# Kernel optimization log

Hardware: AMD Instinct MI355X
Metric: run time of the kernel (lower is better)

## Reference

```python
import jax, jax.numpy as jnp
import numpy as np
from jax import lax

B, D, H, W, C = 2, 144, 64, 160, 32
P = 300000
EPS = 1e-4   # scn BatchNormLeakyReLU default eps
LEAK = 0.2


def setup_inputs() -> dict:
    key = jax.random.key(0)
    ks = jax.random.split(key, 10)
    features = jax.random.normal(ks[0], (P, C), jnp.float32)
    b = jax.random.randint(ks[1], (P, 1), 0, B)
    x = jax.random.randint(ks[2], (P, 1), 0, D)
    y = jax.random.randint(ks[3], (P, 1), 0, H)
    z = jax.random.randint(ks[4], (P, 1), 0, W)
    coords = jnp.concatenate([b, x, y, z], axis=1).astype(jnp.int32)

    def conv_w(k, cin, cout):
        return jax.random.normal(k, (2, 2, 2, cin, cout), jnp.float32) / np.float32(np.sqrt(8 * cin))

    return {
        "features": features, "coords": coords,
        "w1": conv_w(ks[5], C, 64),  "g1": jnp.ones((64,), jnp.float32),  "b1": jnp.zeros((64,), jnp.float32),
        "w2": conv_w(ks[6], 64, 96), "g2": jnp.ones((96,), jnp.float32),  "b2": jnp.zeros((96,), jnp.float32),
        "w3": conv_w(ks[7], 96, 128),"g3": jnp.ones((128,), jnp.float32), "b3": jnp.zeros((128,), jnp.float32),
        "w4": conv_w(ks[8], 128, 1),
    }


def _densify(features, coords):
    # scn.InputLayer mode=4: average features of duplicate coordinates.
    lin = ((coords[:, 0] * D + coords[:, 1]) * H + coords[:, 2]) * W + coords[:, 3]
    grid = jnp.zeros((B * D * H * W, C), features.dtype).at[lin].add(features)
    cnt = jnp.zeros((B * D * H * W,), features.dtype).at[lin].add(1.0)
    grid = grid / jnp.maximum(cnt, 1.0)[:, None]
    x = grid.reshape(B, D, H, W, C)
    mask = (cnt > 0).astype(features.dtype).reshape(B, D, H, W, 1)
    return x, mask


def _conv2s2(x, w):
    # scn.Convolution(dim=3, filter=2, stride=2, bias=False): inactive inputs are zero,
    # so dense VALID conv reproduces values at active output sites exactly.
    return lax.conv_general_dilated(x, w, (2, 2, 2), 'VALID',
                                    dimension_numbers=('NDHWC', 'DHWIO', 'NDHWC'))


def _downsample_mask(mask):
    # Output site is active iff any input in its 2x2x2 window is active.
    return lax.reduce_window(mask, 0.0, lax.max, (1, 2, 2, 2, 1), (1, 2, 2, 2, 1), 'VALID')


def _block(x, mask, w, gamma, beta):
    x = _conv2s2(x, w)
    mask = _downsample_mask(mask)
    n = jnp.maximum(jnp.sum(mask), 1.0)
    # x is exactly zero at inactive sites, so sums over all sites == sums over active sites.
    mean = jnp.sum(x, axis=(0, 1, 2, 3)) / n
    var = jnp.sum(x * x, axis=(0, 1, 2, 3)) / n - mean * mean
    y = (x - mean) * (gamma * lax.rsqrt(var + EPS)) + beta
    y = jnp.where(y > 0, y, LEAK * y) * mask   # LeakyReLU on active sites, zero elsewhere
    return y, mask


def reference(features, coords, w1, g1, b1, w2, g2, b2, w3, g3, b3, w4):
    x, mask = _densify(features, coords)
    x, mask = _block(x, mask, w1, g1, b1)
    x, mask = _block(x, mask, w2, g2, b2)
    x, mask = _block(x, mask, w3, g3, b3)
    x = _conv2s2(x, w4)                 # [B, 9, 4, 10, 1]
    mask = _downsample_mask(mask)
    return jax.nn.sigmoid(x) * mask     # sigmoid of features; inactive sites zeroed
```

## Files before the change

kernel.cpp:

```cpp
#include <hip/hip_runtime.h>
#include <math.h>

#define PNUM 300000
#define B_ 2
#define D0 144
#define H0 64
#define W0 160
#define NVOX (B_*D0*H0*W0)

#define D1 72
#define H1 32
#define W1 80
#define N1S (B_*D1*H1*W1)

#define D2 36
#define H2 16
#define W2 40
#define N2S (B_*D2*H2*W2)

#define D3 18
#define H3 8
#define W3 20
#define N3S (B_*D3*H3*W3)

#define D4 9
#define H4 4
#define W4 10
#define N4S (B_*D4*H4*W4)

#define EPS_ 1e-4f
#define LEAK_ 0.2f

typedef __attribute__((ext_vector_type(8))) short v8s;
typedef __attribute__((ext_vector_type(4))) float v4f;

typedef unsigned short ushort_t;
typedef unsigned int uint_t;
typedef unsigned long long ull_t;

__device__ __forceinline__ ushort_t f2b(float f) {
  union { float f; uint_t u; } x; x.f = f;
  uint_t r = x.u + 0x7FFFu + ((x.u >> 16) & 1u);
  return (ushort_t)(r >> 16);
}
__device__ __forceinline__ float b2f(ushort_t h) {
  union { uint_t u; float f; } x; x.u = ((uint_t)h) << 16; return x.f;
}
__device__ __forceinline__ uint_t bn2(uint_t w, float s0, float h0, float s1, float h1,
                                      float msk) {
  float v0 = b2f((ushort_t)(w & 0xffff));
  float v1 = b2f((ushort_t)(w >> 16));
  v0 = fmaf(v0, s0, h0); v1 = fmaf(v1, s1, h1);
  v0 = fmaxf(v0, LEAK_ * v0) * msk;
  v1 = fmaxf(v1, LEAK_ * v1) * msk;
  return (uint_t)f2b(v0) | ((uint_t)f2b(v1) << 16);
}

#define OFF_CNT     0
#define OFF_STATS   2949120
#define OFF_START   2965504
#define OFF_SORTED  5914624
#define OFF_AKLIST  6214624
#define OFF_WT1     6514624
#define OFF_WT2     6522816
#define OFF_WT3     6555584
#define OFF_AFEATB  6621120
#define OFF_X1B     11421120
#define OFF_X2B     23217600
#define OFF_X3B     26166720
#define OFF_M1      26535360
#define OFF_M2      26904000
#define OFF_M3      26950080

#define ST_S1P  0
#define ST_Q1P  2560
#define ST_S2P  5120
#define ST_Q2P  7424
#define ST_S3P  9728
#define ST_Q3P  12032
#define ST_N2P  14336
#define ST_N3P  14368
#define ST_GCUR 14400
#define ST_PK   14404

__device__ __forceinline__ int voxkey(int b, int x, int y, int z) {
  int p = ((b*D1 + (x >> 1))*H1 + (y >> 1))*W1 + (z >> 1);
  int oct = ((x & 1) << 2) | ((y & 1) << 1) | (z & 1);
  return p*8 + oct;
}

__global__ __launch_bounds__(256) void k_count(const int* __restrict__ coords,
                                               int* __restrict__ cnt) {
  int i = blockIdx.x * 256 + threadIdx.x;
  if (i >= PNUM) return;
  int4 c = *(const int4*)(coords + i*4);
  atomicAdd(&cnt[voxkey(c.x, c.y, c.z, c.w)], 1);
}

__global__ __launch_bounds__(1024) void k_alloc(const int* __restrict__ cnt,
                                                int* __restrict__ start,
                                                int* __restrict__ cursor,
                                                int* __restrict__ gcur) {
  __shared__ int wsum[16];
  __shared__ int blockBase;
  int t = threadIdx.x;
  int idx0 = blockIdx.x * 16384 + t * 16;
  int c[16];
  int tsum = 0;
#pragma unroll
  for (int j = 0; j < 4; j++) {
    int4 cv = *(const int4*)(cnt + idx0 + j*4);
    c[j*4+0] = cv.x; c[j*4+1] = cv.y; c[j*4+2] = cv.z; c[j*4+3] = cv.w;
    tsum += cv.x + cv.y + cv.z + cv.w;
  }
  int lane = t & 63, wid = t >> 6;
  int incl = tsum;
#pragma unroll
  for (int off = 1; off < 64; off <<= 1) {
    int v = __shfl_up(incl, off);
    if (lane >= off) incl += v;
  }
  if (lane == 63) wsum[wid] = incl;
  __syncthreads();
  if (t == 0) {
    int tot = 0;
#pragma unroll
    for (int w = 0; w < 16; w++) { int v = wsum[w]; wsum[w] = tot; tot += v; }
    blockBase = atomicAdd(gcur, tot);
  }
  __syncthreads();
  int st = blockBase + wsum[wid] + incl - tsum;
#pragma unroll
  for (int j = 0; j < 4; j++) {
    int4 sv;
    sv.x = st; st += c[j*4+0];
    sv.y = st; st += c[j*4+1];
    sv.z = st; st += c[j*4+2];
    sv.w = st; st += c[j*4+3];
    *(int4*)(start + idx0 + j*4) = sv;
    *(int4*)(cursor + idx0 + j*4) = sv;
  }
}

__global__ __launch_bounds__(256) void k_scatter(const int* __restrict__ coords,
                                                 int* __restrict__ cursor,
                                                 int* __restrict__ sorted) {
  int i = blockIdx.x * 256 + threadIdx.x;
  if (i >= PNUM) return;
  int4 c = *(const int4*)(coords + i*4);
  int slot = atomicAdd(&cursor[voxkey(c.x, c.y, c.z, c.w)], 1);
  sorted[slot] = i;
}

__global__ __launch_bounds__(1024) void k_plist(const int* __restrict__ cnt,
                                                float* __restrict__ m1,
                                                int* __restrict__ aklist,
                                                ull_t* __restrict__ pkctr) {
  __shared__ int wsum[16];
  __shared__ ull_t sbase;
  int t = threadIdx.x;
  int p0 = blockIdx.x * 4096 + t * 4;
  int lane = t & 63, wid = t >> 6;
  uint_t mb[4];
  int packed = 0;
#pragma unroll
  for (int j = 0; j < 4; j++) {
    const int4* c4 = (const int4*)(cnt + (size_t)(p0 + j)*8);
    int4 a = c4[0], b = c4[1];
    uint_t m = 0;
    m |= (a.x > 0) ? 1u : 0; m |= (a.y > 0) ? 2u : 0;
    m |= (a.z > 0) ? 4u : 0; m |= (a.w > 0) ? 8u : 0;
    m |= (b.x > 0) ? 16u : 0; m |= (b.y > 0) ? 32u : 0;
    m |= (b.z > 0) ? 64u : 0; m |= (b.w > 0) ? 128u : 0;
    mb[j] = m;
    int ck = __popc(m);
    int pa = (ck > 0) ? 1 : 0;
    m1[p0 + j] = pa ? 1.f : 0.f;
    packed += (pa << 16) | ck;
  }
  int incl = packed;
#pragma unroll
  for (int o = 1; o < 64; o <<= 1) {
    int v = __shfl_up(incl, o);
    if (lane >= o) incl += v;
  }
  if (lane == 63) wsum[wid] = incl;
  __syncthreads();
  if (t == 0) {
    int tot = 0;
#pragma unroll
    for (int w = 0; w < 16; w++) { int v = wsum[w]; wsum[w] = tot; tot += v; }
    ull_t add = ((ull_t)(uint_t)(tot >> 16) << 32) | (ull_t)(uint_t)(tot & 0xffff);
    sbase = atomicAdd(pkctr, add);
  }
  __syncthreads();
  ull_t base = sbase;
  int excl = wsum[wid] + incl - packed;
  int koff = (int)(base & 0xffffffffULL) + (excl & 0xffff);
#pragma unroll
  for (int j = 0; j < 4; j++) {
    uint_t m = mb[j];
    while (m) {
      int i = __ffs(m) - 1; m &= m - 1;
      aklist[koff++] = (p0 + j)*8 + i;
    }
  }
}

__global__ __launch_bounds__(256) void k_avg(const float* __restrict__ feat,
                                             const int* __restrict__ sorted,
                                             const int* __restrict__ cnt,
                                             const int* __restrict__ start,
                                             const int* __restrict__ aklist,
                                             const int* __restrict__ nactk,
                                             ushort_t* __restrict__ afb) {
  int gid = blockIdx.x * 256 + threadIdx.x;
  int j = gid >> 3;
  if (j >= nactk[0]) return;
  int key = aklist[j];
  int c = cnt[key];
  int s0 = start[key];
  int q = (gid & 7) * 4;
  float4 acc = {0.f, 0.f, 0.f, 0.f};
  for (int i = 0; i < c; i++) {
    float4 v = *(const float4*)(feat + (size_t)sorted[s0 + i] * 32 + q);
    acc.x += v.x; acc.y += v.y; acc.z += v.z; acc.w += v.w;
  }
  float inv = 1.f / (float)c;
  uint2 o;
  o.x = (uint_t)f2b(acc.x*inv) | ((uint_t)f2b(acc.y*inv) << 16);
  o.y = (uint_t)f2b(acc.z*inv) | ((uint_t)f2b(acc.w*inv) << 16);
  *(uint2*)(afb + (size_t)s0 * 32 + q) = o;
}

__global__ __launch_bounds__(256) void k_prepw(const float* __restrict__ w1,
                                               const float* __restrict__ w2,
                                               const float* __restrict__ w3,
                                               ushort_t* __restrict__ wt1,
                                               ushort_t* __restrict__ wt2,
                                               ushort_t* __restrict__ wt3) {
  int idx = blockIdx.x * 256 + threadIdx.x;
  if (idx < 16384) {
    int c = idx >> 11, r = idx & 2047;
    int co = r >> 5, kk = r & 31;
    wt1[idx] = f2b(w1[(c*32 + kk)*64 + co]);
  } else if (idx < 16384 + 65536) {
    int i = idx - 16384;
    int c = i >> 12, r = i & 4095;
    int co = r >> 5, kk = r & 31;
    int k = c*32 + kk;
    wt2[i] = (co < 96) ? f2b(w2[k*96 + co]) : 0;
  } else if (idx < 16384 + 65536 + 131072) {
    int i = idx - 81920;
    int c = i >> 12, r = i & 4095;
    int co = r >> 5, kk = r & 31;
    int k = c*32 + kk;
    int ch = k >> 7, ci = k & 127;
    wt3[i] = (ci < 96) ? f2b(w3[(ch*96 + ci)*128 + co]) : 0;
  }
}

__global__ __launch_bounds__(256) void k_conv1m(
    const ushort_t* __restrict__ afb, const int* __restrict__ cnt,
    const int* __restrict__ start, const ushort_t* __restrict__ wtg,
    ushort_t* __restrict__ x1b, float* __restrict__ sp, float* __restrict__ qp) {
  __shared__ __align__(16) ushort_t wlds[16384];
  __shared__ int cst[128*9];
  __shared__ float redS[4][64], redQ[4][64];
  int t = threadIdx.x;
#pragma unroll
  for (int i = 0; i < 8; i++)
    ((uint4*)wlds)[t + i*256] = ((const uint4*)wtg)[t + i*256];
  if (t < 128) {
    int p = blockIdx.x * 128 + t;
    const int4* cp = (const int4*)(cnt + (size_t)p*8);
    const int4* spt = (const int4*)(start + (size_t)p*8);
    int4 c0 = cp[0], c1 = cp[1], s0 = spt[0], s1 = spt[1];
    cst[t*9 + 0] = (c0.x > 0) ? s0.x : -1;
    cst[t*9 + 1] = (c0.y > 0) ? s0.y : -1;
    cst[t*9 + 2] = (c0.z > 0) ? s0.z : -1;
    cst[t*9 + 3] = (c0.w > 0) ? s0.w : -1;
    cst[t*9 + 4] = (c1.x > 0) ? s1.x : -1;
    cst[t*9 + 5] = (c1.y > 0) ? s1.y : -1;
    cst[t*9 + 6] = (c1.z > 0) ? s1.z : -1;
    cst[t*9 + 7] = (c1.w > 0) ? s1.w : -1;
  }
  __syncthreads();
  int lane = t & 63, wv = t >> 6;
  int l15 = lane & 15, q = lane >> 4;
  int SB = wv * 32;
  v8s a[8][2];
#pragma unroll
  for (int c = 0; c < 8; c++) {
#pragma unroll
    for (int mt = 0; mt < 2; mt++) {
      int site = SB + mt*16 + l15;
      int sp2 = cst[site*9 + c];
      v8s av = {0,0,0,0,0,0,0,0};
      if (sp2 >= 0) av = *(const v8s*)(afb + (size_t)sp2*32 + q*8);
      a[c][mt] = av;
    }
  }
  v4f acc[2][4];
#pragma unroll
  for (int i = 0; i < 2; i++)
#pragma unroll
    for (int j = 0; j < 4; j++) acc[i][j] = (v4f){0.f, 0.f, 0.f, 0.f};
#pragma unroll
  for (int c = 0; c < 8; c++) {
    v8s b[4];
#pragma unroll
    for (int nt = 0; nt < 4; nt++)
      b[nt] = *(const v8s*)&wlds[c*2048 + (nt*16 + l15)*32 + q*8];
#pragma unroll
    for (int mt = 0; mt < 2; mt++)
#pragma unroll
      for (int nt = 0; nt < 4; nt++)
        acc[mt][nt] = __builtin_amdgcn_mfma_f32_16x16x32_bf16(a[c][mt], b[nt], acc[mt][nt], 0, 0, 0);
  }
  int pbase = blockIdx.x * 128;
  float ss[4] = {0,0,0,0}, sq[4] = {0,0,0,0};
#pragma unroll
  for (int mt = 0; mt < 2; mt++) {
#pragma unroll
    for (int nt = 0; nt < 4; nt++) {
#pragma unroll
      for (int r = 0; r < 4; r++) {
        int sl = SB + mt*16 + q*4 + r;
        ushort_t h = f2b(acc[mt][nt][r]);
        float v = b2f(h);
        x1b[(size_t)(pbase + sl)*64 + nt*16 + l15] = h;
        ss[nt] += v; sq[nt] += v*v;
      }
    }
  }
#pragma unroll
  for (int nt = 0; nt < 4; nt++) {
    float v1 = ss[nt], v2 = sq[nt];
    v1 += __shfl_xor(v1, 16); v1 += __shfl_xor(v1, 32);
    v2 += __shfl_xor(v2, 16); v2 += __shfl_xor(v2, 32);
    if (lane < 16) { redS[wv][nt*16 + l15] = v1; redQ[wv][nt*16 + l15] = v2; }
  }
  __syncthreads();
  if (t < 64) {
    float s = redS[0][t] + redS[1][t] + redS[2][t] + redS[3][t];
    float qq = redQ[0][t] + redQ[1][t] + redQ[2][t] + redQ[3][t];
    int row = (blockIdx.x & 31) * 80;
    atomicAdd(&sp[row + t], s);
    atomicAdd(&qp[row + t], qq);
  }
}

template <int CSTRIDE, int CIN_REAL, bool NINT, int NROW, int INSTR,
          int DO, int HO, int WO, int DP, int HP, int WP>
__global__ __launch_bounds__(256) void k_convm(
    const ushort_t* __restrict__ xin, const float* __restrict__ mprev,
    const ushort_t* __restrict__ wtg,
    const float* __restrict__ gam, const float* __restrict__ bet,
    const float* __restrict__ spin, const float* __restrict__ qpin,
    const void* __restrict__ ncnt, const float* __restrict__ npin,
    ushort_t* __restrict__ xout, float* __restrict__ osum, float* __restrict__ osq,
    float* __restrict__ mout, float* __restrict__ npart) {
  const int NCHUNK = CSTRIDE / 4;
  __shared__ __align__(16) float sc[CSTRIDE], sh[CSTRIDE];
  __shared__ int   cbase[64*9];
  __shared__ float cmask[64*9];
  __shared__ float redS[4][64], redQ[4][64];
  int t = threadIdx.x;
  if (t < CSTRIDE) {
    float scv = 0.f, shv = 0.f;
    if (t < CIN_REAL) {
      float n;
      if (NINT) n = fmaxf((float)((const int*)ncnt)[0], 1.0f);
      else {
        float nn = 0.f;
        for (int r = 0; r < 32; r++) nn += npin[r];
        n = fmaxf(nn, 1.0f);
      }
      float s1 = 0.f, q1 = 0.f;
      for (int r = 0; r < NROW; r++) { s1 += spin[r*INSTR + t]; q1 += qpin[r*INSTR + t]; }
      float mean = s1 / n;
      float var = q1 / n - mean * mean;
      float s = gam[t] * rsqrtf(var + EPS_);
      scv = s; shv = bet[t] - mean * s;
    }
    sc[t] = scv; sh[t] = shv;
  }
#pragma unroll
  for (int ii = 0; ii < 2; ii++) {
    int idx = t + ii*256;
    int s = idx >> 3, ch = idx & 7;
    int g = blockIdx.x * 64 + s;
    int b = g / (DO*HO*WO); int r = g - b*(DO*HO*WO);
    int ox = r / (HO*WO); r -= ox*(HO*WO);
    int oy = r / WO; int oz = r - oy*WO;
    int ps = ((b*DP + 2*ox + ((ch >> 2) & 1))*HP + 2*oy + ((ch >> 1) & 1))*WP + 2*oz + (ch & 1);
    cbase[s*9 + ch] = ps * CSTRIDE;
    cmask[s*9 + ch] = mprev[ps];
  }
  __syncthreads();
  int lane = t & 63, wv = t >> 6;
  int l15 = lane & 15, q = lane >> 4;
  int SB = (wv & 1) * 32, NB = (wv >> 1) * 64;
  v4f acc[2][4];
#pragma unroll
  for (int i = 0; i < 2; i++)
#pragma unroll
    for (int j = 0; j < 4; j++) acc[i][j] = (v4f){0.f, 0.f, 0.f, 0.f};
  uint4 rawN[2]; float mskN[2]; v8s bN[4];
#pragma unroll
  for (int mt = 0; mt < 2; mt++) {
    int site = SB + mt*16 + l15;
    rawN[mt] = *(const uint4*)(xin + (size_t)cbase[site*9] + q*8);
    mskN[mt] = cmask[site*9];
  }
#pragma unroll
  for (int nt = 0; nt < 4; nt++)
    bN[nt] = *(const v8s*)(wtg + (NB + nt*16 + l15)*32 + q*8);
#pragma unroll
  for (int c = 0; c < NCHUNK; c++) {
    uint4 raw[2] = {rawN[0], rawN[1]};
    float mskc[2] = {mskN[0], mskN[1]};
    v8s b[4] = {bN[0], bN[1], bN[2], bN[3]};
    if (c + 1 < NCHUNK) {
      int ch1 = ((c+1) * 32) / CSTRIDE;
      int cio1 = ((c+1) * 32) % CSTRIDE + q * 8;
#pragma unroll
      for (int mt = 0; mt < 2; mt++) {
        int site = SB + mt*16 + l15;
        rawN[mt] = *(const uint4*)(xin + (size_t)cbase[site*9 + ch1] + cio1);
        mskN[mt] = cmask[site*9 + ch1];
      }
#pragma unroll
      for (int nt = 0; nt < 4; nt++)
        bN[nt] = *(const v8s*)(wtg + (size_t)(c+1)*4096 + (NB + nt*16 + l15)*32 + q*8);
    }
    int cio = (c * 32) % CSTRIDE + q * 8;
    float4 sc0 = *(const float4*)&sc[cio];
    float4 sc1 = *(const float4*)&sc[cio + 4];
    float4 sh0 = *(const float4*)&sh[cio];
    float4 sh1 = *(const float4*)&sh[cio + 4];
    v8s a[2];
#pragma unroll
    for (int mt = 0; mt < 2; mt++) {
      int4 pk;
      pk.x = (int)bn2(raw[mt].x, sc0.x, sh0.x, sc0.y, sh0.y, mskc[mt]);
      pk.y = (int)bn2(raw[mt].y, sc0.z, sh0.z, sc0.w, sh0.w, mskc[mt]);
      pk.z = (int)bn2(raw[mt].z, sc1.x, sh1.x, sc1.y, sh1.y, mskc[mt]);
      pk.w = (int)bn2(raw[mt].w, sc1.z, sh1.z, sc1.w, sh1.w, mskc[mt]);
      a[mt] = *(v8s*)&pk;
    }
#pragma unroll
    for (int mt = 0; mt < 2; mt++)
#pragma unroll
      for (int nt = 0; nt < 4; nt++)
        acc[mt][nt] = __builtin_amdgcn_mfma_f32_16x16x32_bf16(a[mt], b[nt], acc[mt][nt], 0, 0, 0);
  }
  float ss[4] = {0,0,0,0}, sq[4] = {0,0,0,0};
#pragma unroll
  for (int mt = 0; mt < 2; mt++) {
#pragma unroll
    for (int nt = 0; nt < 4; nt++) {
#pragma unroll
      for (int r = 0; r < 4; r++) {
        int sl = SB + mt*16 + q*4 + r;
        size_t gsite = (size_t)blockIdx.x * 64 + sl;
        ushort_t h = f2b(acc[mt][nt][r]);
        float v = b2f(h);
        xout[gsite*128 + NB + nt*16 + l15] = h;
        ss[nt] += v; sq[nt] += v*v;
      }
    }
  }
  if (t < 64) {
    bool act = false;
#pragma unroll
    for (int ch = 0; ch < 8; ch++) act |= (cmask[t*9 + ch] > 0.f);
    mout[blockIdx.x * 64 + t] = act ? 1.f : 0.f;
    unsigned long long bal = __ballot(act);
    if (t == 0) atomicAdd(&npart[blockIdx.x & 31], (float)__popcll(bal));
  }
#pragma unroll
  for (int nt = 0; nt < 4; nt++) {
    float v1 = ss[nt], v2 = sq[nt];
    v1 += __shfl_xor(v1, 16); v1 += __shfl_xor(v1, 32);
    v2 += __shfl_xor(v2, 16); v2 += __shfl_xor(v2, 32);
    if (lane < 16) { redS[wv][nt*16 + l15] = v1; redQ[wv][nt*16 + l15] = v2; }
  }
  __syncthreads();
  if (t < 128) {
    float s, qq;
    if (t < 64) { s = redS[0][t] + redS[1][t]; qq = redQ[0][t] + redQ[1][t]; }
    else        { s = redS[2][t-64] + redS[3][t-64]; qq = redQ[2][t-64] + redQ[3][t-64]; }
    int row = (blockIdx.x & 15) * 144;
    atomicAdd(&osum[row + t], s);
    atomicAdd(&osq[row + t], qq);
  }
}

__global__ __launch_bounds__(256) void k_final(
    const ushort_t* __restrict__ x3b, const float* __restrict__ m3,
    const float* __restrict__ w4, const float* __restrict__ gam,
    const float* __restrict__ bet, const float* __restrict__ spin,
    const float* __restrict__ qpin, const float* __restrict__ npin,
    float* __restrict__ out) {
  __shared__ float sc[128], sh[128];
  __shared__ int cb[8];
  __shared__ float msk[8];
  __shared__ float red[256];
  int t = threadIdx.x;
  if (t < 128) {
    float nn = 0.f;
    for (int r = 0; r < 32; r++) nn += npin[r];
    float n = fmaxf(nn, 1.0f);
    float s1 = 0.f, q1 = 0.f;
    for (int r = 0; r < 16; r++) { s1 += spin[r*144 + t]; q1 += qpin[r*144 + t]; }
    float mean = s1 / n;
    float var = q1 / n - mean * mean;
    float s = gam[t] * rsqrtf(var + EPS_);
    sc[t] = s; sh[t] = bet[t] - mean * s;
  }
  int g = blockIdx.x;
  int b = g / (D4*H4*W4); int r = g - b*(D4*H4*W4);
  int ox = r / (H4*W4); r -= ox*(H4*W4);
  int oy = r / W4; int oz = r - oy*W4;
  if (t < 8) {
    int ps = ((b*D3 + 2*ox + ((t >> 2) & 1))*H3 + 2*oy + ((t >> 1) & 1))*W3 + 2*oz + (t & 1);
    cb[t] = ps * 128;
    msk[t] = m3[ps];
  }
  __syncthreads();
  float acc = 0.f;
#pragma unroll
  for (int ii = 0; ii < 4; ii++) {
    int k = t + ii*256;
    int ch = k >> 7, ci = k & 127;
    float v = b2f(x3b[cb[ch] + ci]);
    v = v * sc[ci] + sh[ci];
    v = (v > 0.f ? v : LEAK_ * v) * msk[ch];
    acc += v * w4[k];
  }
  red[t] = acc;
  __syncthreads();
  if (t < 128) red[t] += red[t + 128];
  __syncthreads();
  if (t < 64) {
    float v = red[t] + red[t + 64];
#pragma unroll
    for (int off = 32; off > 0; off >>= 1) v += __shfl_down(v, off);
    if (t == 0) {
      float any = (msk[0] + msk[1] + msk[2] + msk[3] + msk[4] + msk[5] + msk[6] + msk[7]) > 0.f ? 1.f : 0.f;
      out[g] = any / (1.0f + expf(-v));
    }
  }
}

extern "C" void kernel_launch(void* const* d_in, const int* in_sizes, int n_in,
                              void* d_out, int out_size, void* d_ws, size_t ws_size,
                              hipStream_t stream) {
  (void)in_sizes; (void)n_in; (void)out_size; (void)ws_size;
  const float* feat = (const float*)d_in[0];
  const int*   crd  = (const int*)d_in[1];
  const float* w1 = (const float*)d_in[2];
  const float* g1 = (const float*)d_in[3];
  const float* b1 = (const float*)d_in[4];
  const float* w2 = (const float*)d_in[5];
  const float* g2 = (const float*)d_in[6];
  const float* b2 = (const float*)d_in[7];
  const float* w3 = (const float*)d_in[8];
  const float* g3 = (const float*)d_in[9];
  const float* b3 = (const float*)d_in[10];
  const float* w4 = (const float*)d_in[11];
  float* out = (float*)d_out;
  float* ws  = (float*)d_ws;

  int*      cnt    = (int*)(ws + OFF_CNT);
  float*    st     = ws + OFF_STATS;
  int*      start  = (int*)(ws + OFF_START);
  int*      sorted = (int*)(ws + OFF_SORTED);
  int*      aklist = (int*)(ws + OFF_AKLIST);
  ushort_t* wt1g   = (ushort_t*)(ws + OFF_WT1);
  ushort_t* wt2g   = (ushort_t*)(ws + OFF_WT2);
  ushort_t* wt3g   = (ushort_t*)(ws + OFF_WT3);
  ushort_t* afb    = (ushort_t*)(ws + OFF_AFEATB);
  ushort_t* x1b    = (ushort_t*)(ws + OFF_X1B);
  int*      cursor = (int*)(ws + OFF_X1B);
  ushort_t* x2b    = (ushort_t*)(ws + OFF_X2B);
  ushort_t* x3b    = (ushort_t*)(ws + OFF_X3B);
  float*    m1     = ws + OFF_M1;
  float*    m2     = ws + OFF_M2;
  float*    m3     = ws + OFF_M3;
  ull_t*    pkctr  = (ull_t*)(st + ST_PK);
  int*      nactk  = (int*)(st + ST_PK);
  int*      nactp  = (int*)(st + ST_PK + 1);

  hipMemsetAsync(d_ws, 0, (size_t)(OFF_STATS + 16384) * sizeof(float), stream);

  k_count<<<(PNUM + 255) / 256, 256, 0, stream>>>(crd, cnt);
  k_alloc<<<NVOX / 16384, 1024, 0, stream>>>(cnt, start, cursor, (int*)(st + ST_GCUR));
  k_scatter<<<(PNUM + 255) / 256, 256, 0, stream>>>(crd, cursor, sorted);
  k_plist<<<N1S / 4096, 1024, 0, stream>>>(cnt, m1, aklist, pkctr);
  k_avg<<<(PNUM * 8) / 256 + 1, 256, 0, stream>>>(feat, sorted, cnt, start, aklist,
                                                  nactk, afb);
  k_prepw<<<(16384 + 65536 + 131072) / 256, 256, 0, stream>>>(w1, w2, w3, wt1g, wt2g, wt3g);
  k_conv1m<<<N1S / 128, 256, 0, stream>>>(afb, cnt, start, wt1g, x1b,
                                          st + ST_S1P, st + ST_Q1P);
  k_convm<64, 64, true, 32, 80, D2,H2,W2, D1,H1,W1><<<N2S / 64, 256, 0, stream>>>(
      x1b, m1, wt2g, g1, b1, st + ST_S1P, st + ST_Q1P, (const void*)nactp, nullptr,
      x2b, st + ST_S2P, st + ST_Q2P, m2, st + ST_N2P);
  k_convm<128, 96, false, 16, 144, D3,H3,W3, D2,H2,W2><<<N3S / 64, 256, 0, stream>>>(
      x2b, m2, wt3g, g2, b2, st + ST_S2P, st + ST_Q2P, nullptr, st + ST_N2P,
      x3b, st + ST_S3P, st + ST_Q3P, m3, st + ST_N3P);
  k_final<<<N4S, 256, 0, stream>>>(x3b, m3, w4, g3, b3,
                                   st + ST_S3P, st + ST_Q3P, st + ST_N3P, out);
}
```

Before: 255.8 us.

## Store intermediate grids in octant-blocked order and fuse front-end kernels

Each level's output is now written in octant-blocked (Morton-like) order, so the next conv's 2x2x2 window inputs sit contiguously. That removes the per-site index division and gathered base computation, and makes the input loads contiguous. The active-list build is folded into the allocation scan, count/weight-prep/stats-zeroing are merged into one launch, and the start array is dropped in favour of cursor minus count. The cost is scattered output stores through okey remapping and a 64-bit packed scan in k_alloc.

```diff
diff --git a/kernel.cpp b/kernel.cpp
--- a/kernel.cpp
+++ b/kernel.cpp
@@ -56,9 +56,18 @@
   return (uint_t)f2b(v0) | ((uint_t)f2b(v1) << 16);
 }
 
+template <int DD, int HH, int WW>
+__device__ __forceinline__ int okey(int p) {
+  int b = p / (DD*HH*WW); int r = p - b*(DD*HH*WW);
+  int x = r / (HH*WW); r -= x*(HH*WW);
+  int y = r / WW; int z = r - y*WW;
+  return (((((b*(DD/2) + (x >> 1))*(HH/2) + (y >> 1))*(WW/2)) + (z >> 1)) << 3)
+         | ((x & 1) << 2) | ((y & 1) << 1) | (z & 1);
+}
+
 #define OFF_CNT     0
 #define OFF_STATS   2949120
-#define OFF_START   2965504
+#define OFF_CURSOR  2965504
 #define OFF_SORTED  5914624
 #define OFF_AKLIST  6214624
 #define OFF_WT1     6514624
@@ -89,20 +98,57 @@
   return p*8 + oct;
 }
 
-__global__ __launch_bounds__(256) void k_count(const int* __restrict__ coords,
-                                               int* __restrict__ cnt) {
-  int i = blockIdx.x * 256 + threadIdx.x;
-  if (i >= PNUM) return;
-  int4 c = *(const int4*)(coords + i*4);
-  atomicAdd(&cnt[voxkey(c.x, c.y, c.z, c.w)], 1);
+#define NB_COUNT 1172
+#define NB_PREPW 832
+#define NB_STZ   16
+__global__ __launch_bounds__(256) void k_front(
+    const int* __restrict__ coords, int* __restrict__ cnt,
+    const float* __restrict__ w1, const float* __restrict__ w2,
+    const float* __restrict__ w3,
+    ushort_t* __restrict__ wt1, ushort_t* __restrict__ wt2,
+    ushort_t* __restrict__ wt3, float* __restrict__ stz) {
+  int bb = blockIdx.x, t = threadIdx.x;
+  if (bb < NB_COUNT) {
+    int i = bb * 256 + t;
+    if (i < PNUM) {
+      int4 c = *(const int4*)(coords + i*4);
+      atomicAdd(&cnt[voxkey(c.x, c.y, c.z, c.w)], 1);
+    }
+  } else if (bb < NB_COUNT + NB_PREPW) {
+    int idx = (bb - NB_COUNT) * 256 + t;
+    if (idx < 16384) {
+      int c = idx >> 11, r = idx & 2047;
+      int co = r >> 5, kk = r & 31;
+      wt1[idx] = f2b(w1[(c*32 + kk)*64 + co]);
+    } else if (idx < 16384 + 65536) {
+      int i = idx - 16384;
+      int c = i >> 12, r = i & 4095;
+      int co = r >> 5, kk = r & 31;
+      int k = c*32 + kk;
+      wt2[i] = (co < 96) ? f2b(w2[k*96 + co]) : 0;
+    } else {
+      int i = idx - 81920;
+      int c = i >> 12, r = i & 4095;
+      int co = r >> 5, kk = r & 31;
+      int k = c*32 + kk;
+      int ch = k >> 7, ci = k & 127;
+      wt3[i] = (ci < 96) ? f2b(w3[(ch*96 + ci)*128 + co]) : 0;
+    }
+  } else {
+    int off = ((bb - NB_COUNT - NB_PREPW) * 256 + t) * 4;
+    *(float4*)(stz + off) = make_float4(0.f, 0.f, 0.f, 0.f);
+  }
 }
 
 __global__ __launch_bounds__(1024) void k_alloc(const int* __restrict__ cnt,
-                                                int* __restrict__ start,
                                                 int* __restrict__ cursor,
-                                                int* __restrict__ gcur) {
-  __shared__ int wsum[16];
-  __shared__ int blockBase;
+                                                float* __restrict__ m1b,
+                                                int* __restrict__ aklist,
+                                                int* __restrict__ gcur,
+                                                ull_t* __restrict__ pkctr) {
+  __shared__ ull_t wsum[16];
+  __shared__ int slotBase;
+  __shared__ ull_t pkBase;
   int t = threadIdx.x;
   int idx0 = blockIdx.x * 16384 + t * 16;
   int c[16];
@@ -113,33 +159,52 @@
     c[j*4+0] = cv.x; c[j*4+1] = cv.y; c[j*4+2] = cv.z; c[j*4+3] = cv.w;
     tsum += cv.x + cv.y + cv.z + cv.w;
   }
+  uint_t m0 = 0, m1m = 0;
+#pragma unroll
+  for (int j = 0; j < 8; j++) { if (c[j] > 0) m0 |= (1u << j); }
+#pragma unroll
+  for (int j = 0; j < 8; j++) { if (c[8+j] > 0) m1m |= (1u << j); }
+  int ck = __popc(m0) + __popc(m1m);
+  int pa = ((m0 != 0) ? 1 : 0) + ((m1m != 0) ? 1 : 0);
+  ull_t sv = ((ull_t)(uint_t)tsum << 32) | (ull_t)(uint_t)((pa << 16) | ck);
   int lane = t & 63, wid = t >> 6;
-  int incl = tsum;
-#pragma unroll
-  for (int off = 1; off < 64; off <<= 1) {
-    int v = __shfl_up(incl, off);
-    if (lane >= off) incl += v;
+  ull_t incl = sv;
+#pragma unroll
+  for (int o = 1; o < 64; o <<= 1) {
+    ull_t v = __shfl_up(incl, o);
+    if (lane >= o) incl += v;
   }
   if (lane == 63) wsum[wid] = incl;
   __syncthreads();
   if (t == 0) {
-    int tot = 0;
-#pragma unroll
-    for (int w = 0; w < 16; w++) { int v = wsum[w]; wsum[w] = tot; tot += v; }
-    blockBase = atomicAdd(gcur, tot);
-  }
-  __syncthreads();
-  int st = blockBase + wsum[wid] + incl - tsum;
+    ull_t tot = 0;
+#pragma unroll
+    for (int w = 0; w < 16; w++) { ull_t v = wsum[w]; wsum[w] = tot; tot += v; }
+    slotBase = atomicAdd(gcur, (int)(tot >> 32));
+    uint_t pk = (uint_t)(tot & 0xffffffffULL);
+    pkBase = atomicAdd(pkctr, ((ull_t)(pk >> 16) << 32) | (ull_t)(pk & 0xffff));
+  }
+  __syncthreads();
+  ull_t excl = wsum[wid] + incl - sv;
+  int st = slotBase + (int)(excl >> 32);
+  uint_t pkl = (uint_t)(excl & 0xffffffffULL);
+  int koff = (int)(pkBase & 0xffffffffULL) + (int)(pkl & 0xffff);
 #pragma unroll
   for (int j = 0; j < 4; j++) {
-    int4 sv;
-    sv.x = st; st += c[j*4+0];
-    sv.y = st; st += c[j*4+1];
-    sv.z = st; st += c[j*4+2];
-    sv.w = st; st += c[j*4+3];
-    *(int4*)(start + idx0 + j*4) = sv;
-    *(int4*)(cursor + idx0 + j*4) = sv;
-  }
+    int4 sv2;
+    sv2.x = st; st += c[j*4+0];
+    sv2.y = st; st += c[j*4+1];
+    sv2.z = st; st += c[j*4+2];
+    sv2.w = st; st += c[j*4+3];
+    *(int4*)(cursor + idx0 + j*4) = sv2;
+  }
+  int p0 = idx0 >> 3;
+  m1b[okey<D1,H1,W1>(p0)]     = (m0 != 0) ? 1.f : 0.f;
+  m1b[okey<D1,H1,W1>(p0 + 1)] = (m1m != 0) ? 1.f : 0.f;
+  uint_t m = m0;
+  while (m) { int i = __ffs(m) - 1; m &= m - 1; aklist[koff++] = p0*8 + i; }
+  m = m1m;
+  while (m) { int i = __ffs(m) - 1; m &= m - 1; aklist[koff++] = (p0 + 1)*8 + i; }
 }
 
 __global__ __launch_bounds__(256) void k_scatter(const int* __restrict__ coords,
@@ -152,65 +217,10 @@
   sorted[slot] = i;
 }
 
-__global__ __launch_bounds__(1024) void k_plist(const int* __restrict__ cnt,
-                                                float* __restrict__ m1,
-                                                int* __restrict__ aklist,
-                                                ull_t* __restrict__ pkctr) {
-  __shared__ int wsum[16];
-  __shared__ ull_t sbase;
-  int t = threadIdx.x;
-  int p0 = blockIdx.x * 4096 + t * 4;
-  int lane = t & 63, wid = t >> 6;
-  uint_t mb[4];
-  int packed = 0;
-#pragma unroll
-  for (int j = 0; j < 4; j++) {
-    const int4* c4 = (const int4*)(cnt + (size_t)(p0 + j)*8);
-    int4 a = c4[0], b = c4[1];
-    uint_t m = 0;
-    m |= (a.x > 0) ? 1u : 0; m |= (a.y > 0) ? 2u : 0;
-    m |= (a.z > 0) ? 4u : 0; m |= (a.w > 0) ? 8u : 0;
-    m |= (b.x > 0) ? 16u : 0; m |= (b.y > 0) ? 32u : 0;
-    m |= (b.z > 0) ? 64u : 0; m |= (b.w > 0) ? 128u : 0;
-    mb[j] = m;
-    int ck = __popc(m);
-    int pa = (ck > 0) ? 1 : 0;
-    m1[p0 + j] = pa ? 1.f : 0.f;
-    packed += (pa << 16) | ck;
-  }
-  int incl = packed;
-#pragma unroll
-  for (int o = 1; o < 64; o <<= 1) {
-    int v = __shfl_up(incl, o);
-    if (lane >= o) incl += v;
-  }
-  if (lane == 63) wsum[wid] = incl;
-  __syncthreads();
-  if (t == 0) {
-    int tot = 0;
-#pragma unroll
-    for (int w = 0; w < 16; w++) { int v = wsum[w]; wsum[w] = tot; tot += v; }
-    ull_t add = ((ull_t)(uint_t)(tot >> 16) << 32) | (ull_t)(uint_t)(tot & 0xffff);
-    sbase = atomicAdd(pkctr, add);
-  }
-  __syncthreads();
-  ull_t base = sbase;
-  int excl = wsum[wid] + incl - packed;
-  int koff = (int)(base & 0xffffffffULL) + (excl & 0xffff);
-#pragma unroll
-  for (int j = 0; j < 4; j++) {
-    uint_t m = mb[j];
-    while (m) {
-      int i = __ffs(m) - 1; m &= m - 1;
-      aklist[koff++] = (p0 + j)*8 + i;
-    }
-  }
-}
-
 __global__ __launch_bounds__(256) void k_avg(const float* __restrict__ feat,
                                              const int* __restrict__ sorted,
                                              const int* __restrict__ cnt,
-                                             const int* __restrict__ start,
+                                             const int* __restrict__ cursor,
                                              const int* __restrict__ aklist,
                                              const int* __restrict__ nactk,
                                              ushort_t* __restrict__ afb) {
@@ -219,7 +229,7 @@
   if (j >= nactk[0]) return;
   int key = aklist[j];
   int c = cnt[key];
-  int s0 = start[key];
+  int s0 = cursor[key] - c;
   int q = (gid & 7) * 4;
   float4 acc = {0.f, 0.f, 0.f, 0.f};
   for (int i = 0; i < c; i++) {
@@ -233,39 +243,13 @@
   *(uint2*)(afb + (size_t)s0 * 32 + q) = o;
 }
 
-__global__ __launch_bounds__(256) void k_prepw(const float* __restrict__ w1,
-                                               const float* __restrict__ w2,
-                                               const float* __restrict__ w3,
-                                               ushort_t* __restrict__ wt1,
-                                               ushort_t* __restrict__ wt2,
-                                               ushort_t* __restrict__ wt3) {
-  int idx = blockIdx.x * 256 + threadIdx.x;
-  if (idx < 16384) {
-    int c = idx >> 11, r = idx & 2047;
-    int co = r >> 5, kk = r & 31;
-    wt1[idx] = f2b(w1[(c*32 + kk)*64 + co]);
-  } else if (idx < 16384 + 65536) {
-    int i = idx - 16384;
-    int c = i >> 12, r = i & 4095;
-    int co = r >> 5, kk = r & 31;
-    int k = c*32 + kk;
-    wt2[i] = (co < 96) ? f2b(w2[k*96 + co]) : 0;
-  } else if (idx < 16384 + 65536 + 131072) {
-    int i = idx - 81920;
-    int c = i >> 12, r = i & 4095;
-    int co = r >> 5, kk = r & 31;
-    int k = c*32 + kk;
-    int ch = k >> 7, ci = k & 127;
-    wt3[i] = (ci < 96) ? f2b(w3[(ch*96 + ci)*128 + co]) : 0;
-  }
-}
-
 __global__ __launch_bounds__(256) void k_conv1m(
     const ushort_t* __restrict__ afb, const int* __restrict__ cnt,
-    const int* __restrict__ start, const ushort_t* __restrict__ wtg,
+    const int* __restrict__ cursor, const ushort_t* __restrict__ wtg,
     ushort_t* __restrict__ x1b, float* __restrict__ sp, float* __restrict__ qp) {
   __shared__ __align__(16) ushort_t wlds[16384];
   __shared__ int cst[128*9];
+  __shared__ int okl[128];
   __shared__ float redS[4][64], redQ[4][64];
   int t = threadIdx.x;
 #pragma unroll
@@ -273,17 +257,18 @@
     ((uint4*)wlds)[t + i*256] = ((const uint4*)wtg)[t + i*256];
   if (t < 128) {
     int p = blockIdx.x * 128 + t;
+    okl[t] = okey<D1,H1,W1>(p);
     const int4* cp = (const int4*)(cnt + (size_t)p*8);
-    const int4* spt = (const int4*)(start + (size_t)p*8);
-    int4 c0 = cp[0], c1 = cp[1], s0 = spt[0], s1 = spt[1];
-    cst[t*9 + 0] = (c0.x > 0) ? s0.x : -1;
-    cst[t*9 + 1] = (c0.y > 0) ? s0.y : -1;
-    cst[t*9 + 2] = (c0.z > 0) ? s0.z : -1;
-    cst[t*9 + 3] = (c0.w > 0) ? s0.w : -1;
-    cst[t*9 + 4] = (c1.x > 0) ? s1.x : -1;
-    cst[t*9 + 5] = (c1.y > 0) ? s1.y : -1;
-    cst[t*9 + 6] = (c1.z > 0) ? s1.z : -1;
-    cst[t*9 + 7] = (c1.w > 0) ? s1.w : -1;
+    const int4* up = (const int4*)(cursor + (size_t)p*8);
+    int4 c0 = cp[0], c1 = cp[1], u0 = up[0], u1 = up[1];
+    cst[t*9 + 0] = (c0.x > 0) ? (u0.x - c0.x) : -1;
+    cst[t*9 + 1] = (c0.y > 0) ? (u0.y - c0.y) : -1;
+    cst[t*9 + 2] = (c0.z > 0) ? (u0.z - c0.z) : -1;
+    cst[t*9 + 3] = (c0.w > 0) ? (u0.w - c0.w) : -1;
+    cst[t*9 + 4] = (c1.x > 0) ? (u1.x - c1.x) : -1;
+    cst[t*9 + 5] = (c1.y > 0) ? (u1.y - c1.y) : -1;
+    cst[t*9 + 6] = (c1.z > 0) ? (u1.z - c1.z) : -1;
+    cst[t*9 + 7] = (c1.w > 0) ? (u1.w - c1.w) : -1;
   }
   __syncthreads();
   int lane = t & 63, wv = t >> 6;
@@ -318,7 +303,6 @@
       for (int nt = 0; nt < 4; nt++)
         acc[mt][nt] = __builtin_amdgcn_mfma_f32_16x16x32_bf16(a[c][mt], b[nt], acc[mt][nt], 0, 0, 0);
   }
-  int pbase = blockIdx.x * 128;
   float ss[4] = {0,0,0,0}, sq[4] = {0,0,0,0};
 #pragma unroll
   for (int mt = 0; mt < 2; mt++) {
@@ -329,7 +313,7 @@
         int sl = SB + mt*16 + q*4 + r;
         ushort_t h = f2b(acc[mt][nt][r]);
         float v = b2f(h);
-        x1b[(size_t)(pbase + sl)*64 + nt*16 + l15] = h;
+        x1b[(size_t)okl[sl]*64 + nt*16 + l15] = h;
         ss[nt] += v; sq[nt] += v*v;
       }
     }
@@ -352,7 +336,7 @@
 }
 
 template <int CSTRIDE, int CIN_REAL, bool NINT, int NROW, int INSTR,
-          int DO, int HO, int WO, int DP, int HP, int WP>
+          int DO, int HO, int WO>
 __global__ __launch_bounds__(256) void k_convm(
     const ushort_t* __restrict__ xin, const float* __restrict__ mprev,
     const ushort_t* __restrict__ wtg,
@@ -363,8 +347,8 @@
     float* __restrict__ mout, float* __restrict__ npart) {
   const int NCHUNK = CSTRIDE / 4;
   __shared__ __align__(16) float sc[CSTRIDE], sh[CSTRIDE];
-  __shared__ int   cbase[64*9];
   __shared__ float cmask[64*9];
+  __shared__ int okl[64];
   __shared__ float redS[4][64], redQ[4][64];
   int t = threadIdx.x;
   if (t < CSTRIDE) {
@@ -389,19 +373,14 @@
 #pragma unroll
   for (int ii = 0; ii < 2; ii++) {
     int idx = t + ii*256;
-    int s = idx >> 3, ch = idx & 7;
-    int g = blockIdx.x * 64 + s;
-    int b = g / (DO*HO*WO); int r = g - b*(DO*HO*WO);
-    int ox = r / (HO*WO); r -= ox*(HO*WO);
-    int oy = r / WO; int oz = r - oy*WO;
-    int ps = ((b*DP + 2*ox + ((ch >> 2) & 1))*HP + 2*oy + ((ch >> 1) & 1))*WP + 2*oz + (ch & 1);
-    cbase[s*9 + ch] = ps * CSTRIDE;
-    cmask[s*9 + ch] = mprev[ps];
-  }
+    cmask[(idx >> 3)*9 + (idx & 7)] = mprev[(size_t)blockIdx.x * 512 + idx];
+  }
+  if (t < 64) okl[t] = okey<DO,HO,WO>(blockIdx.x * 64 + t);
   __syncthreads();
   int lane = t & 63, wv = t >> 6;
   int l15 = lane & 15, q = lane >> 4;
   int SB = (wv & 1) * 32, NB = (wv >> 1) * 64;
+  size_t gbase = (size_t)blockIdx.x * 512;
   v4f acc[2][4];
 #pragma unroll
   for (int i = 0; i < 2; i++)
@@ -411,7 +390,7 @@
 #pragma unroll
   for (int mt = 0; mt < 2; mt++) {
     int site = SB + mt*16 + l15;
-    rawN[mt] = *(const uint4*)(xin + (size_t)cbase[site*9] + q*8);
+    rawN[mt] = *(const uint4*)(xin + (gbase + site*8) * CSTRIDE + q*8);
     mskN[mt] = cmask[site*9];
   }
 #pragma unroll
@@ -428,7 +407,7 @@
 #pragma unroll
       for (int mt = 0; mt < 2; mt++) {
         int site = SB + mt*16 + l15;
-        rawN[mt] = *(const uint4*)(xin + (size_t)cbase[site*9 + ch1] + cio1);
+        rawN[mt] = *(const uint4*)(xin + (gbase + site*8 + ch1) * CSTRIDE + cio1);
         mskN[mt] = cmask[site*9 + ch1];
       }
 #pragma unroll
@@ -464,10 +443,9 @@
 #pragma unroll
       for (int r = 0; r < 4; r++) {
         int sl = SB + mt*16 + q*4 + r;
-        size_t gsite = (size_t)blockIdx.x * 64 + sl;
         ushort_t h = f2b(acc[mt][nt][r]);
         float v = b2f(h);
-        xout[gsite*128 + NB + nt*16 + l15] = h;
+        xout[(size_t)okl[sl]*128 + NB + nt*16 + l15] = h;
         ss[nt] += v; sq[nt] += v*v;
       }
     }
@@ -476,7 +454,7 @@
     bool act = false;
 #pragma unroll
     for (int ch = 0; ch < 8; ch++) act |= (cmask[t*9 + ch] > 0.f);
-    mout[blockIdx.x * 64 + t] = act ? 1.f : 0.f;
+    mout[okl[t]] = act ? 1.f : 0.f;
     unsigned long long bal = __ballot(act);
     if (t == 0) atomicAdd(&npart[blockIdx.x & 31], (float)__popcll(bal));
   }
@@ -499,13 +477,12 @@
 }
 
 __global__ __launch_bounds__(256) void k_final(
-    const ushort_t* __restrict__ x3b, const float* __restrict__ m3,
+    const ushort_t* __restrict__ x3b, const float* __restrict__ m3b,
     const float* __restrict__ w4, const float* __restrict__ gam,
     const float* __restrict__ bet, const float* __restrict__ spin,
     const float* __restrict__ qpin, const float* __restrict__ npin,
     float* __restrict__ out) {
   __shared__ float sc[128], sh[128];
-  __shared__ int cb[8];
   __shared__ float msk[8];
   __shared__ float red[256];
   int t = threadIdx.x;
@@ -521,21 +498,14 @@
     sc[t] = s; sh[t] = bet[t] - mean * s;
   }
   int g = blockIdx.x;
-  int b = g / (D4*H4*W4); int r = g - b*(D4*H4*W4);
-  int ox = r / (H4*W4); r -= ox*(H4*W4);
-  int oy = r / W4; int oz = r - oy*W4;
-  if (t < 8) {
-    int ps = ((b*D3 + 2*ox + ((t >> 2) & 1))*H3 + 2*oy + ((t >> 1) & 1))*W3 + 2*oz + (t & 1);
-    cb[t] = ps * 128;
-    msk[t] = m3[ps];
-  }
+  if (t < 8) msk[t] = m3b[g*8 + t];
   __syncthreads();
   float acc = 0.f;
 #pragma unroll
   for (int ii = 0; ii < 4; ii++) {
     int k = t + ii*256;
     int ch = k >> 7, ci = k & 127;
-    float v = b2f(x3b[cb[ch] + ci]);
+    float v = b2f(x3b[(size_t)(g*8 + ch)*128 + ci]);
     v = v * sc[ci] + sh[ci];
     v = (v > 0.f ? v : LEAK_ * v) * msk[ch];
     acc += v * w4[k];
@@ -576,7 +546,7 @@
 
   int*      cnt    = (int*)(ws + OFF_CNT);
   float*    st     = ws + OFF_STATS;
-  int*      start  = (int*)(ws + OFF_START);
+  int*      cursor = (int*)(ws + OFF_CURSOR);
   int*      sorted = (int*)(ws + OFF_SORTED);
   int*      aklist = (int*)(ws + OFF_AKLIST);
   ushort_t* wt1g   = (ushort_t*)(ws + OFF_WT1);
@@ -584,33 +554,32 @@
   ushort_t* wt3g   = (ushort_t*)(ws + OFF_WT3);
   ushort_t* afb    = (ushort_t*)(ws + OFF_AFEATB);
   ushort_t* x1b    = (ushort_t*)(ws + OFF_X1B);
-  int*      cursor = (int*)(ws + OFF_X1B);
   ushort_t* x2b    = (ushort_t*)(ws + OFF_X2B);
   ushort_t* x3b    = (ushort_t*)(ws + OFF_X3B);
-  float*    m1     = ws + OFF_M1;
-  float*    m2     = ws + OFF_M2;
-  float*    m3     = ws + OFF_M3;
+  float*    m1b    = ws + OFF_M1;
+  float*    m2b    = ws + OFF_M2;
+  float*    m3b    = ws + OFF_M3;
   ull_t*    pkctr  = (ull_t*)(st + ST_PK);
   int*      nactk  = (int*)(st + ST_PK);
   int*      nactp  = (int*)(st + ST_PK + 1);
 
-  hipMemsetAsync(d_ws, 0, (size_t)(OFF_STATS + 16384) * sizeof(float), stream);
-
-  k_count<<<(PNUM + 255) / 256, 256, 0, stream>>>(crd, cnt);
-  k_alloc<<<NVOX / 16384, 1024, 0, stream>>>(cnt, start, cursor, (int*)(st + ST_GCUR));
+  hipMemsetAsync(cnt, 0, (size_t)NVOX * sizeof(int), stream);
+
+  k_front<<<NB_COUNT + NB_PREPW + NB_STZ, 256, 0, stream>>>(
+      crd, cnt, w1, w2, w3, wt1g, wt2g, wt3g, st);
+  k_alloc<<<NVOX / 16384, 1024, 0, stream>>>(cnt, cursor, m1b, aklist,
+                                             (int*)(st + ST_GCUR), pkctr);
   k_scatter<<<(PNUM + 255) / 256, 256, 0, stream>>>(crd, cursor, sorted);
-  k_plist<<<N1S / 4096, 1024, 0, stream>>>(cnt, m1, aklist, pkctr);
-  k_avg<<<(PNUM * 8) / 256 + 1, 256, 0, stream>>>(feat, sorted, cnt, start, aklist,
+  k_avg<<<(PNUM * 8) / 256 + 1, 256, 0, stream>>>(feat, sorted, cnt, cursor, aklist,
                                                   nactk, afb);
-  k_prepw<<<(16384 + 65536 + 131072) / 256, 256, 0, stream>>>(w1, w2, w3, wt1g, wt2g, wt3g);
-  k_conv1m<<<N1S / 128, 256, 0, stream>>>(afb, cnt, start, wt1g, x1b,
+  k_conv1m<<<N1S / 128, 256, 0, stream>>>(afb, cnt, cursor, wt1g, x1b,
                                           st + ST_S1P, st + ST_Q1P);
-  k_convm<64, 64, true, 32, 80, D2,H2,W2, D1,H1,W1><<<N2S / 64, 256, 0, stream>>>(
-      x1b, m1, wt2g, g1, b1, st + ST_S1P, st + ST_Q1P, (const void*)nactp, nullptr,
-      x2b, st + ST_S2P, st + ST_Q2P, m2, st + ST_N2P);
-  k_convm<128, 96, false, 16, 144, D3,H3,W3, D2,H2,W2><<<N3S / 64, 256, 0, stream>>>(
-      x2b, m2, wt3g, g2, b2, st + ST_S2P, st + ST_Q2P, nullptr, st + ST_N2P,
-      x3b, st + ST_S3P, st + ST_Q3P, m3, st + ST_N3P);
-  k_final<<<N4S, 256, 0, stream>>>(x3b, m3, w4, g3, b3,
+  k_convm<64, 64, true, 32, 80, D2,H2,W2><<<N2S / 64, 256, 0, stream>>>(
+      x1b, m1b, wt2g, g1, b1, st + ST_S1P, st + ST_Q1P, (const void*)nactp, nullptr,
+      x2b, st + ST_S2P, st + ST_Q2P, m2b, st + ST_N2P);
+  k_convm<128, 96, false, 16, 144, D3,H3,W3><<<N3S / 64, 256, 0, stream>>>(
+      x2b, m2b, wt3g, g2, b2, st + ST_S2P, st + ST_Q2P, nullptr, st + ST_N2P,
+      x3b, st + ST_S3P, st + ST_Q3P, m3b, st + ST_N3P);
+  k_final<<<N4S, 256, 0, stream>>>(x3b, m3b, w4, g3, b3,
                                    st + ST_S3P, st + ST_Q3P, st + ST_N3P, out);
 }
```

Result: faster. 245.7 us (-3.9%).
